# Kernel optimization log

Hardware: AMD Instinct MI355X
Metric: run time of the kernel (lower is better)

Reference implementation:

```python
import jax, jax.numpy as jnp
import numpy as np
import math

D = 2048  # hidden_size
B, S = 4, 2048
EPS = 1e-5


def _ln(z, g, b):
    m = jnp.mean(z, axis=-1, keepdims=True)
    v = jnp.mean(jnp.square(z - m), axis=-1, keepdims=True)
    return (z - m) * jax.lax.rsqrt(v + EPS) * g + b


def _rotate_half(x):
    h = x.shape[-1] // 2
    return jnp.concatenate([-x[..., h:], x[..., :h]], axis=-1)


def _mas_normalize(logits):
    m = jnp.max(jnp.abs(logits), axis=-1, keepdims=True)
    return logits / (m + 1e-9)


def setup_inputs() -> dict:
    key = jax.random.key(0)
    ks = jax.random.split(key, 12)
    std = 0.02
    return {
        "x": jax.random.normal(ks[0], (B, S, D), dtype=jnp.float32),
        "position_ids": jnp.arange(S, dtype=jnp.int32),
        "ln1_g": jnp.ones((D,), jnp.float32),
        "ln1_b": jnp.zeros((D,), jnp.float32),
        # stacked params for [q, k, v, o]
        "mu_w": std * jax.random.normal(ks[1], (4, D, D), dtype=jnp.float32),
        "mu_b": jnp.zeros((4, D), jnp.float32),
        "proto_w": std * jax.random.normal(ks[2], (4, D, D), dtype=jnp.float32),
        "gate": jnp.zeros((4, D), jnp.float32),
        "pt_w": std * jax.random.normal(ks[3], (4, D, D), dtype=jnp.float32),
        "pln_g": jnp.ones((4, D), jnp.float32),
        "pln_b": jnp.zeros((4, D), jnp.float32),
        "incoming": std * jax.random.normal(ks[4], (4, D, D), dtype=jnp.float32),
    }


def reference(x, position_ids, ln1_g, ln1_b, mu_w, mu_b, proto_w, gate,
              pt_w, pln_g, pln_b, incoming):
    d = x.shape[-1]
    inv_sqrt_d = 1.0 / math.sqrt(d)

    # proto_state = proto_weight + LN(Linear(incoming))  per module [4, D, D]
    prc = jnp.einsum('nij,noj->nio', incoming, pt_w)
    proto_state = proto_w + _ln(prc, pln_g[:, None, :], pln_b[:, None, :])

    ln1_out = _ln(x, ln1_g, ln1_b)            # [B,S,D]
    ctx = jnp.mean(ln1_out, axis=1)           # [B,D]

    # qkv computation outputs: silu(ln1_out @ mu_w.T + mu_b) for n in {q,k,v}
    comp = jax.nn.silu(jnp.einsum('bsd,nod->nbso', ln1_out, mu_w[:3])
                       + mu_b[:3][:, None, None, :])            # [3,B,S,D]
    # routing from context vector
    match_ctx = jnp.einsum('bd,nod->nbo', ctx, proto_state[:3]) * inv_sqrt_d
    routing = match_ctx + gate[:3][:, None, :]                  # [3,B,D]
    gating = _mas_normalize(routing)
    masked = gating[:, :, None, :] * comp                       # [3,B,S,D]
    q, k, v = masked[0], masked[1], masked[2]

    # RoPE over full hidden dim (num_heads == 1)
    seq = position_ids.shape[0]
    inv_freq = 1.0 / (10000.0 ** (jnp.arange(0, d, 2, dtype=jnp.float32) / d))
    t = jnp.arange(seq, dtype=jnp.float32)
    freqs = t[:, None] * inv_freq[None, :]
    emb = jnp.concatenate([freqs, freqs], axis=-1)              # [S,D]
    cos = jnp.cos(emb)[position_ids]
    sin = jnp.sin(emb)[position_ids]
    q = q * cos + _rotate_half(q) * sin
    k = k * cos + _rotate_half(k) * sin

    # causal single-head attention, scale 1/sqrt(head_dim=D)
    scores = jnp.einsum('bqd,bkd->bqk', q, k) * inv_sqrt_d      # [B,S,S]
    causal = jnp.tril(jnp.ones((seq, seq), dtype=bool))
    scores = jnp.where(causal, scores, jnp.finfo(scores.dtype).min)
    probs = jax.nn.softmax(scores, axis=-1)
    attn_out = jnp.einsum('bqk,bkd->bqd', probs, v)             # [B,S,D]

    # output SPL + routing
    ctx_o = jnp.mean(attn_out, axis=1)
    c_o = jax.nn.silu(jnp.einsum('bsd,od->bso', attn_out, mu_w[3]) + mu_b[3])
    match_o = jnp.einsum('bd,od->bo', ctx_o, proto_state[3]) * inv_sqrt_d
    gating_o = _mas_normalize(match_o + gate[3])
    x_out = x + gating_o[:, None, :] * c_o
    return x_out
```

## Files before the change

kernel.cpp:

```cpp
#include <hip/hip_runtime.h>
#include <hip/hip_bf16.h>

#define Dh 2048
#define Bh 4
#define Sh 2048
#define NROW 8192
#define HALF 1024
#define INV_SQRT_D 0.022097086912079608f
#define LNEPS 1e-5f

typedef __hip_bfloat16 bf16;
typedef short short8 __attribute__((ext_vector_type(8)));
typedef float f32x4 __attribute__((ext_vector_type(4)));

__device__ inline float warp_sum(float x) {
#pragma unroll
  for (int o = 32; o > 0; o >>= 1) x += __shfl_down(x, o);
  return x;
}
__device__ inline float warp_max(float x) {
#pragma unroll
  for (int o = 32; o > 0; o >>= 1) x = fmaxf(x, __shfl_down(x, o));
  return x;
}
__device__ inline float block_sum(float x, float* sm4) {
  x = warp_sum(x);
  int w = threadIdx.x >> 6;
  if ((threadIdx.x & 63) == 0) sm4[w] = x;
  __syncthreads();
  float r = sm4[0] + sm4[1] + sm4[2] + sm4[3];
  __syncthreads();
  return r;
}
__device__ inline float block_max(float x, float* sm4) {
  x = warp_max(x);
  int w = threadIdx.x >> 6;
  if ((threadIdx.x & 63) == 0) sm4[w] = x;
  __syncthreads();
  float r = fmaxf(fmaxf(sm4[0], sm4[1]), fmaxf(sm4[2], sm4[3]));
  __syncthreads();
  return r;
}

__device__ inline void gload_lds16(const void* g, void* lds) {
  __builtin_amdgcn_global_load_lds(
      (const __attribute__((address_space(1))) unsigned int*)(unsigned long long)g,
      (__attribute__((address_space(3))) unsigned int*)(unsigned long long)lds,
      16, 0, 0);
}

#define MM(R, AF)                                                              \
  acc[R][0] = __builtin_amdgcn_mfma_f32_16x16x32_bf16(AF, b0, acc[R][0], 0, 0, 0); \
  acc[R][1] = __builtin_amdgcn_mfma_f32_16x16x32_bf16(AF, b1, acc[R][1], 0, 0, 0); \
  acc[R][2] = __builtin_amdgcn_mfma_f32_16x16x32_bf16(AF, b2, acc[R][2], 0, 0, 0); \
  acc[R][3] = __builtin_amdgcn_mfma_f32_16x16x32_bf16(AF, b3, acc[R][3], 0, 0, 0);

template <int MODE>
__global__ __launch_bounds__(512, 4) void pgemm(
    const bf16* __restrict__ Aall, const bf16* __restrict__ Ball,
    void* __restrict__ Call, int N, int K, int lda, int ldb,
    long sAz, long sBz, long sCz,
    const float* __restrict__ e0, const float* __restrict__ e1,
    const float* __restrict__ e2) {
  const int bm0 = blockIdx.x * 128;
  const int bn0 = blockIdx.y * 256;
  if (MODE == 2 && bn0 > bm0 + 127) return;
  const int z = blockIdx.z;
  const bf16* A = Aall + (long)z * sAz;
  const bf16* B = Ball + (long)z * sBz;

  __shared__ __align__(16) char smem[49152];
  const int tid = threadIdx.x;
  const int l = tid & 63, w = tid >> 6;
  const int wr = w >> 2, wc = w & 3;

  f32x4 acc[4][4] = {};
  const int nt = K >> 5;

  const int sg = (((l & 3) ^ ((l >> 3) & 3)) << 3);
  const int srow = (w << 4) + (l >> 2);
  const bf16* aS  = A + (long)(bm0 + srow) * lda + sg;
  const bf16* bS0 = B + (long)(bn0 + srow) * ldb + sg;
  const bf16* bS1 = B + (long)(bn0 + 128 + srow) * ldb + sg;
  char* const dA = smem + (w << 10);
  char* const dB = smem + 8192 + (w << 10);

  auto stageA = [&](int tt) {
    gload_lds16(aS + (tt << 5), dA + (tt & 1) * 24576);
  };
  auto stageB = [&](int tt) {
    int boff = (tt & 1) * 24576;
    gload_lds16(bS0 + (tt << 5), dB + boff);
    gload_lds16(bS1 + (tt << 5), dB + boff + 8192);
  };

  stageA(0); stageB(0);
  if (nt > 1) stageB(1);
  if (nt > 1) asm volatile("s_waitcnt vmcnt(2)" ::: "memory");
  else        asm volatile("s_waitcnt vmcnt(0)" ::: "memory");
  __builtin_amdgcn_sched_barrier(0);
  asm volatile("s_barrier" ::: "memory");

  const int rslot = (((l >> 4) ^ ((l >> 1) & 3)) << 4);
  const int abyte = (((wr << 6) + (l & 15)) << 6) + rslot;
  const int bbyte = (((wc << 6) + (l & 15)) << 6) + rslot;

  for (int t = 0; t < nt; ++t) {
    const char* Ab = smem + (t & 1) * 24576;
    const char* Bb = Ab + 8192;
    short8 b0 = *(const short8*)(Bb + bbyte);
    short8 b1 = *(const short8*)(Bb + bbyte + 1024);
    short8 b2 = *(const short8*)(Bb + bbyte + 2048);
    short8 b3 = *(const short8*)(Bb + bbyte + 3072);
    short8 a0 = *(const short8*)(Ab + abyte);
    short8 a1 = *(const short8*)(Ab + abyte + 1024);
    if (t + 1 < nt) stageA(t + 1);
    MM(0, a0) MM(1, a1)
    asm volatile("s_waitcnt lgkmcnt(0)" ::: "memory");
    asm volatile("s_barrier" ::: "memory");
    short8 a2 = *(const short8*)(Ab + abyte + 2048);
    short8 a3 = *(const short8*)(Ab + abyte + 3072);
    if (t + 2 < nt) stageB(t + 2);
    MM(2, a2) MM(3, a3)
    if (t < nt - 1) {
      asm volatile("s_waitcnt lgkmcnt(0)" ::: "memory");
      if (t + 2 < nt) asm volatile("s_waitcnt vmcnt(2)" ::: "memory");
      else            asm volatile("s_waitcnt vmcnt(0)" ::: "memory");
      __builtin_amdgcn_sched_barrier(0);
      asm volatile("s_barrier" ::: "memory");
    }
  }

  const int lc = l & 15, lr4 = (l >> 4) << 2;
#pragma unroll
  for (int fr = 0; fr < 4; ++fr) {
    int gr0 = bm0 + (wr << 6) + fr * 16 + lr4;
#pragma unroll
    for (int fc = 0; fc < 4; ++fc) {
      int gc = bn0 + (wc << 6) + fc * 16 + lc;
#pragma unroll
      for (int qv = 0; qv < 4; ++qv) {
        int gr = gr0 + qv;
        float a = acc[fr][fc][qv];
        if (MODE == 0) {
          ((float*)Call + (long)z * sCz)[(long)gr * N + gc] = a;
        } else if (MODE == 1) {
          float val = a + e0[z * Dh + gc];
          float sil = val / (1.f + __expf(-val));
          int bb = gr >> 11;
          float g = e1[(z * Bh + bb) * Dh + gc];
          ((bf16*)Call + (long)z * sCz)[(long)gr * N + gc] =
              __float2bfloat16(sil * g);
        } else if (MODE == 2) {
          ((float*)Call + (long)z * sCz)[(long)gr * N + gc] = a * INV_SQRT_D;
        } else {
          float val = a + e0[gc];
          float sil = val / (1.f + __expf(-val));
          int bb = gr >> 11;
          ((float*)Call)[(long)gr * N + gc] =
              e2[(long)gr * N + gc] + e1[bb * Dh + gc] * sil;
        }
      }
    }
  }
}

__global__ __launch_bounds__(512, 4) void pgemm_h(
    const bf16* __restrict__ Aall, const bf16* __restrict__ Ball,
    bf16* __restrict__ Call, int N, int lda, int ldb,
    long sAz, long sBz, long sCz) {
  const int fid = blockIdx.x;
  const int p = fid >> 8, q = fid & 255;
  const int mh = q >> 5;
  const int z = (q >> 3) & 3, ni = q & 7;
  const int mi = p ? (15 - mh) : mh;
  const int bm0 = mi * 128, bn0 = ni * 256;
  const bf16* A = Aall + (long)z * sAz;
  const bf16* B = Ball + (long)z * sBz;

  __shared__ __align__(16) char smem[49152];
  const int tid = threadIdx.x;
  const int l = tid & 63, w = tid >> 6;
  const int wr = w >> 2, wc = w & 3;
  f32x4 acc[4][4] = {};
  const int nt = (bm0 + 128) >> 5;

  const int sg = (((l & 3) ^ ((l >> 3) & 3)) << 3);
  const int srow = (w << 4) + (l >> 2);
  const bf16* aS  = A + (long)(bm0 + srow) * lda + sg;
  const bf16* bS0 = B + (long)(bn0 + srow) * ldb + sg;
  const bf16* bS1 = B + (long)(bn0 + 128 + srow) * ldb + sg;
  char* const dA = smem + (w << 10);
  char* const dB = smem + 8192 + (w << 10);

  auto stageA = [&](int tt) {
    gload_lds16(aS + (tt << 5), dA + (tt & 1) * 24576);
  };
  auto stageB = [&](int tt) {
    int boff = (tt & 1) * 24576;
    gload_lds16(bS0 + (tt << 5), dB + boff);
    gload_lds16(bS1 + (tt << 5), dB + boff + 8192);
  };

  stageA(0); stageB(0);
  if (nt > 1) stageB(1);
  if (nt > 1) asm volatile("s_waitcnt vmcnt(2)" ::: "memory");
  else        asm volatile("s_waitcnt vmcnt(0)" ::: "memory");
  __builtin_amdgcn_sched_barrier(0);
  asm volatile("s_barrier" ::: "memory");

  const int rslot = (((l >> 4) ^ ((l >> 1) & 3)) << 4);
  const int abyte = (((wr << 6) + (l & 15)) << 6) + rslot;
  const int bbyte = (((wc << 6) + (l & 15)) << 6) + rslot;

  for (int t = 0; t < nt; ++t) {
    const char* Ab = smem + (t & 1) * 24576;
    const char* Bb = Ab + 8192;
    short8 b0 = *(const short8*)(Bb + bbyte);
    short8 b1 = *(const short8*)(Bb + bbyte + 1024);
    short8 b2 = *(const short8*)(Bb + bbyte + 2048);
    short8 b3 = *(const short8*)(Bb + bbyte + 3072);
    short8 a0 = *(const short8*)(Ab + abyte);
    short8 a1 = *(const short8*)(Ab + abyte + 1024);
    if (t + 1 < nt) stageA(t + 1);
    MM(0, a0) MM(1, a1)
    asm volatile("s_waitcnt lgkmcnt(0)" ::: "memory");
    asm volatile("s_barrier" ::: "memory");
    short8 a2 = *(const short8*)(Ab + abyte + 2048);
    short8 a3 = *(const short8*)(Ab + abyte + 3072);
    if (t + 2 < nt) stageB(t + 2);
    MM(2, a2) MM(3, a3)
    if (t < nt - 1) {
      asm volatile("s_waitcnt lgkmcnt(0)" ::: "memory");
      if (t + 2 < nt) asm volatile("s_waitcnt vmcnt(2)" ::: "memory");
      else            asm volatile("s_waitcnt vmcnt(0)" ::: "memory");
      __builtin_amdgcn_sched_barrier(0);
      asm volatile("s_barrier" ::: "memory");
    }
  }

  const int lc = l & 15, lr4 = (l >> 4) << 2;
  bf16* C = Call + (long)z * sCz;
#pragma unroll
  for (int fr = 0; fr < 4; ++fr) {
    int gr0 = bm0 + (wr << 6) + fr * 16 + lr4;
#pragma unroll
    for (int fc = 0; fc < 4; ++fc) {
      int gc = bn0 + (wc << 6) + fc * 16 + lc;
#pragma unroll
      for (int qv = 0; qv < 4; ++qv) {
        C[(long)(gr0 + qv) * N + gc] = __float2bfloat16(acc[fr][fc][qv]);
      }
    }
  }
}

__global__ __launch_bounds__(256) void cvt3_kernel(
    const float* __restrict__ s0, const float* __restrict__ s1,
    const float* __restrict__ s2, bf16* __restrict__ o0, bf16* __restrict__ o1,
    bf16* __restrict__ o2, long n) {
  const float* in = (blockIdx.y == 0) ? s0 : (blockIdx.y == 1) ? s1 : s2;
  bf16* out = (blockIdx.y == 0) ? o0 : (blockIdx.y == 1) ? o1 : o2;
  long i = ((long)blockIdx.x * 256 + threadIdx.x) * 4;
  if (i >= n) return;
  float4 v = *(const float4*)(in + i);
  out[i + 0] = __float2bfloat16(v.x);
  out[i + 1] = __float2bfloat16(v.y);
  out[i + 2] = __float2bfloat16(v.z);
  out[i + 3] = __float2bfloat16(v.w);
}

__global__ __launch_bounds__(256) void transpose_kernel(const bf16* __restrict__ in,
                                                        bf16* __restrict__ out) {
  __shared__ bf16 t[64][65];
  int b = blockIdx.z;
  int s0 = blockIdx.x * 64, d0 = blockIdx.y * 64;
  const bf16* ib = in + (long)b * Sh * Dh;
  bf16* ob = out + (long)b * Sh * Dh;
  int tx = threadIdx.x & 63, ty = threadIdx.x >> 6;
#pragma unroll
  for (int r = ty; r < 64; r += 4) t[r][tx] = ib[(long)(s0 + r) * Dh + d0 + tx];
  __syncthreads();
#pragma unroll
  for (int r = ty; r < 64; r += 4) ob[(long)(d0 + r) * Sh + s0 + tx] = t[tx][r];
}

__global__ __launch_bounds__(256) void ln1_kernel(const float* __restrict__ x,
    const float* __restrict__ g, const float* __restrict__ b, bf16* __restrict__ out) {
  __shared__ float sm4[4];
  long r = blockIdx.x;
  const float* row = x + r * Dh;
  float v[8];
  float s = 0.f, s2 = 0.f;
#pragma unroll
  for (int c = 0; c < 8; ++c) {
    float t = row[threadIdx.x + c * 256];
    v[c] = t; s += t; s2 += t * t;
  }
  s = block_sum(s, sm4);
  s2 = block_sum(s2, sm4);
  float mean = s * (1.f / Dh);
  float rstd = rsqrtf(s2 * (1.f / Dh) - mean * mean + LNEPS);
#pragma unroll
  for (int c = 0; c < 8; ++c) {
    int o = threadIdx.x + c * 256;
    out[r * Dh + o] = __float2bfloat16((v[c] - mean) * rstd * g[o] + b[o]);
  }
}

__global__ __launch_bounds__(256) void meanrow_kernel(const bf16* __restrict__ in,
                                                      float* __restrict__ outbd) {
  int gid = blockIdx.x * 256 + threadIdx.x;
  int s0 = blockIdx.y * 128;
  long base = ((long)(gid >> 11) * Sh + s0) * Dh + (gid & 2047);
  float s = 0.f;
  for (int t = 0; t < 128; ++t) s += __bfloat162float(in[base + (long)t * Dh]);
  atomicAdd(&outbd[gid], s * (1.f / Sh));
}

__global__ __launch_bounds__(256) void route_kernel(
    const float* __restrict__ prc, const float* __restrict__ proto_w,
    const float* __restrict__ pln_g, const float* __restrict__ pln_b,
    const float* __restrict__ gate, const float* __restrict__ ctx,
    float* __restrict__ routing, float* __restrict__ ps3) {
  __shared__ float sm4[4];
  int i = blockIdx.x, n = blockIdx.y;
  long rb = ((long)n * Dh + i) * Dh;
  float v[8];
  float s = 0.f, s2 = 0.f;
#pragma unroll
  for (int c = 0; c < 8; ++c) {
    float t = prc[rb + threadIdx.x + c * 256];
    v[c] = t; s += t; s2 += t * t;
  }
  s = block_sum(s, sm4);
  s2 = block_sum(s2, sm4);
  float mean = s * (1.f / Dh);
  float rstd = rsqrtf(s2 * (1.f / Dh) - mean * mean + LNEPS);
  if (n == 3) {
#pragma unroll
    for (int c = 0; c < 8; ++c) {
      int o = threadIdx.x + c * 256;
      float ps = proto_w[rb + o] + (v[c] - mean) * rstd * pln_g[3 * Dh + o] + pln_b[3 * Dh + o];
      ps3[(long)i * Dh + o] = ps;
    }
  } else {
    float acc[4] = {0.f, 0.f, 0.f, 0.f};
#pragma unroll
    for (int c = 0; c < 8; ++c) {
      int o = threadIdx.x + c * 256;
      float ps = proto_w[rb + o] + (v[c] - mean) * rstd * pln_g[n * Dh + o] + pln_b[n * Dh + o];
#pragma unroll
      for (int b = 0; b < 4; ++b) acc[b] += ps * ctx[b * Dh + o];
    }
    for (int b = 0; b < 4; ++b) {
      float r = block_sum(acc[b], sm4);
      if (threadIdx.x == 0)
        routing[(n * 4 + b) * Dh + i] = r * INV_SQRT_D + gate[n * Dh + i];
    }
  }
}

__global__ __launch_bounds__(256) void route_o_kernel(
    const float* __restrict__ ps3, const float* __restrict__ ctxo,
    const float* __restrict__ gate, float* __restrict__ routing) {
  __shared__ float sm4[4];
  int i = blockIdx.x;
  float acc[4] = {0.f, 0.f, 0.f, 0.f};
#pragma unroll
  for (int c = 0; c < 8; ++c) {
    int o = threadIdx.x + c * 256;
    float p = ps3[(long)i * Dh + o];
#pragma unroll
    for (int b = 0; b < 4; ++b) acc[b] += p * ctxo[b * Dh + o];
  }
  for (int b = 0; b < 4; ++b) {
    float r = block_sum(acc[b], sm4);
    if (threadIdx.x == 0)
      routing[(12 + b) * Dh + i] = r * INV_SQRT_D + gate[3 * Dh + i];
  }
}

__global__ __launch_bounds__(256) void masnorm_kernel(const float* __restrict__ rin,
                                                      float* __restrict__ gout) {
  __shared__ float sm4[4];
  long r = blockIdx.x;
  float m = 0.f;
#pragma unroll
  for (int c = 0; c < 8; ++c)
    m = fmaxf(m, fabsf(rin[r * Dh + threadIdx.x + c * 256]));
  m = block_max(m, sm4);
  float inv = 1.f / (m + 1e-9f);
#pragma unroll
  for (int c = 0; c < 8; ++c) {
    int o = threadIdx.x + c * 256;
    gout[r * Dh + o] = rin[r * Dh + o] * inv;
  }
}

__global__ __launch_bounds__(256) void rope_table_kernel(float* __restrict__ cosT,
                                                         float* __restrict__ sinT) {
  int idx = blockIdx.x * 256 + threadIdx.x;
  int t = idx >> 10, f = idx & 1023;
  float inv_freq = expf(-(float)f * (9.210340371976184f / 1024.f));
  float ang = (float)t * inv_freq;
  cosT[idx] = cosf(ang);
  sinT[idx] = sinf(ang);
}

__global__ __launch_bounds__(256) void rope_kernel(bf16* __restrict__ q, bf16* __restrict__ k,
    const int* __restrict__ pos, const float* __restrict__ cosT,
    const float* __restrict__ sinT) {
  long r = blockIdx.x;
  int s = (int)(r & (Sh - 1));
  int p = pos[s];
#pragma unroll
  for (int c = 0; c < 4; ++c) {
    int t = threadIdx.x + c * 256;
    float cv = cosT[(long)p * HALF + t];
    float sv = sinT[(long)p * HALF + t];
    long i1 = r * Dh + t, i2 = i1 + HALF;
    float q1 = __bfloat162float(q[i1]), q2 = __bfloat162float(q[i2]);
    q[i1] = __float2bfloat16(q1 * cv - q2 * sv);
    q[i2] = __float2bfloat16(q2 * cv + q1 * sv);
    float k1 = __bfloat162float(k[i1]), k2 = __bfloat162float(k[i2]);
    k[i1] = __float2bfloat16(k1 * cv - k2 * sv);
    k[i2] = __float2bfloat16(k2 * cv + k1 * sv);
  }
}

__global__ __launch_bounds__(256) void softmax_kernel(const float* __restrict__ scores,
                                                      bf16* __restrict__ probs) {
  __shared__ float buf[Sh];
  __shared__ float sm4[4];
  long r = blockIdx.x;
  int qi = (int)(r & (Sh - 1));
  const float* row = scores + r * (long)Sh;
  bf16* prow = probs + r * (long)Sh;
  int n = qi + 1;
  float m = -3.0e38f;
  for (int o = threadIdx.x; o < n; o += 256) {
    float x = row[o]; buf[o] = x; m = fmaxf(m, x);
  }
  m = block_max(m, sm4);
  float s = 0.f;
  for (int o = threadIdx.x; o < n; o += 256) {
    float e = __expf(buf[o] - m); buf[o] = e; s += e;
  }
  s = block_sum(s, sm4);
  float inv = 1.f / s;
  for (int o = threadIdx.x; o < n; o += 256) prow[o] = __float2bfloat16(buf[o] * inv);
  for (int o = n + (int)threadIdx.x; o < Sh; o += 256) prow[o] = __float2bfloat16(0.f);
}

extern "C" void kernel_launch(void* const* d_in, const int* in_sizes, int n_in,
                              void* d_out, int out_size, void* d_ws, size_t ws_size,
                              hipStream_t stream) {
  const float* x       = (const float*)d_in[0];
  const int*   pos     = (const int*)d_in[1];
  const float* ln1_g   = (const float*)d_in[2];
  const float* ln1_b   = (const float*)d_in[3];
  const float* mu_w    = (const float*)d_in[4];
  const float* mu_b    = (const float*)d_in[5];
  const float* proto_w = (const float*)d_in[6];
  const float* gate    = (const float*)d_in[7];
  const float* pt_w    = (const float*)d_in[8];
  const float* pln_g   = (const float*)d_in[9];
  const float* pln_b   = (const float*)d_in[10];
  const float* incoming= (const float*)d_in[11];

  char* w = (char*)d_ws;
  const long BF = 33554432L;
  bf16*  ln1    = (bf16*)(w);
  bf16*  qb     = (bf16*)(w + BF);
  bf16*  kb     = (bf16*)(w + 2 * BF);
  bf16*  vb     = (bf16*)(w + 3 * BF);
  bf16*  attn   = (bf16*)(w + 4 * BF);
  bf16*  mu_wb  = (bf16*)(w + 5 * BF);
  bf16*  ptw_b  = (bf16*)(w + 6 * BF);
  bf16*  vT     = ptw_b;
  bf16*  inc_b  = (bf16*)(w + 7 * BF);
  bf16*  probs  = inc_b;
  float* ps3    = (float*)(w + 8 * BF);
  float* cosT   = (float*)(w + 8 * BF + 16777216L);
  float* sinT   = cosT + (long)Sh * HALF;
  float* ctx    = sinT + (long)Sh * HALF;
  float* ctxo   = ctx + Bh * Dh;
  float* routing= ctxo + Bh * Dh;
  float* gating = routing + 16 * Dh;
  float* scores = (float*)d_out;

  const long DD4 = 4L * Dh * Dh;

  hipMemsetAsync(ctx, 0, 2L * Bh * Dh * sizeof(float), stream);

  rope_table_kernel<<<(Sh * HALF) / 256, 256, 0, stream>>>(cosT, sinT);
  cvt3_kernel<<<dim3(DD4 / 1024, 3), 256, 0, stream>>>(
      mu_w, incoming, pt_w, mu_wb, inc_b, ptw_b, DD4);
  ln1_kernel<<<NROW, 256, 0, stream>>>(x, ln1_g, ln1_b, ln1);
  meanrow_kernel<<<dim3(32, 16), 256, 0, stream>>>(ln1, ctx);
  pgemm<0><<<dim3(16, 8, 4), 512, 0, stream>>>(
      inc_b, ptw_b, scores, Dh, Dh, Dh, Dh,
      (long)Dh * Dh, (long)Dh * Dh, (long)Dh * Dh, nullptr, nullptr, nullptr);
  route_kernel<<<dim3(Dh, 4), 256, 0, stream>>>(scores, proto_w, pln_g, pln_b,
                                                gate, ctx, routing, ps3);
  masnorm_kernel<<<12, 256, 0, stream>>>(routing, gating);
  pgemm<1><<<dim3(64, 8, 3), 512, 0, stream>>>(
      ln1, mu_wb, qb, Dh, Dh, Dh, Dh,
      0L, (long)Dh * Dh, (long)NROW * Dh, mu_b, gating, nullptr);
  rope_kernel<<<NROW, 256, 0, stream>>>(qb, kb, pos, cosT, sinT);
  pgemm<2><<<dim3(16, 8, 4), 512, 0, stream>>>(
      qb, kb, scores, Sh, Dh, Dh, Dh,
      (long)Sh * Dh, (long)Sh * Dh, (long)Sh * Sh, nullptr, nullptr, nullptr);
  softmax_kernel<<<Bh * Sh, 256, 0, stream>>>(scores, probs);
  transpose_kernel<<<dim3(32, 32, 4), 256, 0, stream>>>(vb, vT);
  pgemm_h<<<512, 512, 0, stream>>>(
      probs, vT, attn, Dh, Sh, Sh,
      (long)Sh * Sh, (long)Dh * Sh, (long)Sh * Dh);
  meanrow_kernel<<<dim3(32, 16), 256, 0, stream>>>(attn, ctxo);
  route_o_kernel<<<Dh, 256, 0, stream>>>(ps3, ctxo, gate, routing);
  masnorm_kernel<<<4, 256, 0, stream>>>(routing + 12 * Dh, gating + 12 * Dh);
  pgemm<4><<<dim3(64, 8, 1), 512, 0, stream>>>(
      attn, mu_wb + 3L * Dh * Dh, d_out, Dh, Dh, Dh, Dh,
      0L, 0L, 0L, mu_b + 3 * Dh, gating + 12 * Dh, x);
}
```

Before: 710.3 us.

## Fuse RoPE into QKV GEMM epilogue, widen warp tiles, store scores as fp16

```diff
diff --git a/kernel.cpp b/kernel.cpp
--- a/kernel.cpp
+++ b/kernel.cpp
@@ -1,5 +1,6 @@
 #include <hip/hip_runtime.h>
 #include <hip/hip_bf16.h>
+#include <hip/hip_fp16.h>
 
 #define Dh 2048
 #define Bh 4
@@ -56,14 +57,17 @@
   acc[R][3] = __builtin_amdgcn_mfma_f32_16x16x32_bf16(AF, b3, acc[R][3], 0, 0, 0);
 
 template <int MODE>
-__global__ __launch_bounds__(512, 4) void pgemm(
+__global__ __launch_bounds__(256, 2) void pgemm(
     const bf16* __restrict__ Aall, const bf16* __restrict__ Ball,
     void* __restrict__ Call, int N, int K, int lda, int ldb,
     long sAz, long sBz, long sCz,
     const float* __restrict__ e0, const float* __restrict__ e1,
-    const float* __restrict__ e2) {
+    const float* __restrict__ e2,
+    const int* __restrict__ pos, const float* __restrict__ cosT,
+    const float* __restrict__ sinT) {
   const int bm0 = blockIdx.x * 128;
   const int bn0 = blockIdx.y * 256;
+  const int ns = blockIdx.y;
   if (MODE == 2 && bn0 > bm0 + 127) return;
   const int z = blockIdx.z;
   const bf16* A = Aall + (long)z * sAz;
@@ -71,38 +75,50 @@
 
   __shared__ __align__(16) char smem[49152];
   const int tid = threadIdx.x;
-  const int l = tid & 63, w = tid >> 6;
-  const int wr = w >> 2, wc = w & 3;
-
-  f32x4 acc[4][4] = {};
+  const int l = tid & 63, wc = tid >> 6;
+
+  f32x4 acc[8][4] = {};
   const int nt = K >> 5;
 
   const int sg = (((l & 3) ^ ((l >> 3) & 3)) << 3);
-  const int srow = (w << 4) + (l >> 2);
-  const bf16* aS  = A + (long)(bm0 + srow) * lda + sg;
-  const bf16* bS0 = B + (long)(bn0 + srow) * ldb + sg;
-  const bf16* bS1 = B + (long)(bn0 + 128 + srow) * ldb + sg;
-  char* const dA = smem + (w << 10);
-  char* const dB = smem + 8192 + (w << 10);
+  const int lrow = l >> 2;
+  const bf16* aP0 = A + (long)(bm0 + (wc << 4) + lrow) * lda + sg;
+  const bf16* aP1 = aP0 + 64L * lda;
+  const bf16* bP[4];
+#pragma unroll
+  for (int j = 0; j < 4; ++j) {
+    int colbase;
+    if (MODE == 1)
+      colbase = (((wc >> 1) & 1) << 10) + (ns << 7) + (j << 5) + ((wc & 1) << 4);
+    else
+      colbase = bn0 + (wc << 4) + (j << 6);
+    bP[j] = B + (long)(colbase + lrow) * ldb + sg;
+  }
+  char* const dA = smem + (wc << 10);
+  char* const dB = smem + 8192 + (wc << 10);
 
   auto stageA = [&](int tt) {
-    gload_lds16(aS + (tt << 5), dA + (tt & 1) * 24576);
+    int boff = (tt & 1) * 24576;
+    gload_lds16(aP0 + (tt << 5), dA + boff);
+    gload_lds16(aP1 + (tt << 5), dA + boff + 4096);
   };
   auto stageB = [&](int tt) {
     int boff = (tt & 1) * 24576;
-    gload_lds16(bS0 + (tt << 5), dB + boff);
-    gload_lds16(bS1 + (tt << 5), dB + boff + 8192);
+    gload_lds16(bP[0] + (tt << 5), dB + boff);
+    gload_lds16(bP[1] + (tt << 5), dB + boff + 4096);
+    gload_lds16(bP[2] + (tt << 5), dB + boff + 8192);
+    gload_lds16(bP[3] + (tt << 5), dB + boff + 12288);
   };
 
   stageA(0); stageB(0);
   if (nt > 1) stageB(1);
-  if (nt > 1) asm volatile("s_waitcnt vmcnt(2)" ::: "memory");
+  if (nt > 1) asm volatile("s_waitcnt vmcnt(4)" ::: "memory");
   else        asm volatile("s_waitcnt vmcnt(0)" ::: "memory");
   __builtin_amdgcn_sched_barrier(0);
   asm volatile("s_barrier" ::: "memory");
 
   const int rslot = (((l >> 4) ^ ((l >> 1) & 3)) << 4);
-  const int abyte = (((wr << 6) + (l & 15)) << 6) + rslot;
+  const int abyte = ((l & 15) << 6) + rslot;
   const int bbyte = (((wc << 6) + (l & 15)) << 6) + rslot;
 
   for (int t = 0; t < nt; ++t) {
@@ -114,17 +130,21 @@
     short8 b3 = *(const short8*)(Bb + bbyte + 3072);
     short8 a0 = *(const short8*)(Ab + abyte);
     short8 a1 = *(const short8*)(Ab + abyte + 1024);
+    short8 a2 = *(const short8*)(Ab + abyte + 2048);
+    short8 a3 = *(const short8*)(Ab + abyte + 3072);
     if (t + 1 < nt) stageA(t + 1);
-    MM(0, a0) MM(1, a1)
+    MM(0, a0) MM(1, a1) MM(2, a2) MM(3, a3)
     asm volatile("s_waitcnt lgkmcnt(0)" ::: "memory");
     asm volatile("s_barrier" ::: "memory");
-    short8 a2 = *(const short8*)(Ab + abyte + 2048);
-    short8 a3 = *(const short8*)(Ab + abyte + 3072);
+    short8 a4 = *(const short8*)(Ab + abyte + 4096);
+    short8 a5 = *(const short8*)(Ab + abyte + 5120);
+    short8 a6 = *(const short8*)(Ab + abyte + 6144);
+    short8 a7 = *(const short8*)(Ab + abyte + 7168);
     if (t + 2 < nt) stageB(t + 2);
-    MM(2, a2) MM(3, a3)
+    MM(4, a4) MM(5, a5) MM(6, a6) MM(7, a7)
     if (t < nt - 1) {
       asm volatile("s_waitcnt lgkmcnt(0)" ::: "memory");
-      if (t + 2 < nt) asm volatile("s_waitcnt vmcnt(2)" ::: "memory");
+      if (t + 2 < nt) asm volatile("s_waitcnt vmcnt(4)" ::: "memory");
       else            asm volatile("s_waitcnt vmcnt(0)" ::: "memory");
       __builtin_amdgcn_sched_barrier(0);
       asm volatile("s_barrier" ::: "memory");
@@ -133,39 +153,72 @@
 
   const int lc = l & 15, lr4 = (l >> 4) << 2;
 #pragma unroll
-  for (int fr = 0; fr < 4; ++fr) {
-    int gr0 = bm0 + (wr << 6) + fr * 16 + lr4;
-#pragma unroll
-    for (int fc = 0; fc < 4; ++fc) {
-      int gc = bn0 + (wc << 6) + fc * 16 + lc;
+  for (int fr = 0; fr < 8; ++fr) {
+    int gr0 = bm0 + fr * 16 + lr4;
+    if (MODE == 1) {
+      int gcs[4];
+#pragma unroll
+      for (int fc = 0; fc < 4; ++fc)
+        gcs[fc] = ((fc >> 1) << 10) + (ns << 7) + (wc << 5) + ((fc & 1) << 4) + lc;
+      int chi0 = (ns << 7) + (wc << 5) + lc;
 #pragma unroll
       for (int qv = 0; qv < 4; ++qv) {
         int gr = gr0 + qv;
-        float a = acc[fr][fc][qv];
-        if (MODE == 0) {
-          ((float*)Call + (long)z * sCz)[(long)gr * N + gc] = a;
-        } else if (MODE == 1) {
-          float val = a + e0[z * Dh + gc];
+        int s = gr & (Sh - 1);
+        int bb = gr >> 11;
+        float msk[4];
+#pragma unroll
+        for (int fc = 0; fc < 4; ++fc) {
+          float val = acc[fr][fc][qv] + e0[z * Dh + gcs[fc]];
           float sil = val / (1.f + __expf(-val));
-          int bb = gr >> 11;
-          float g = e1[(z * Bh + bb) * Dh + gc];
-          ((bf16*)Call + (long)z * sCz)[(long)gr * N + gc] =
-              __float2bfloat16(sil * g);
-        } else if (MODE == 2) {
-          ((float*)Call + (long)z * sCz)[(long)gr * N + gc] = a * INV_SQRT_D;
+          msk[fc] = sil * e1[(z * Bh + bb) * Dh + gcs[fc]];
+        }
+        float out[4];
+        if (z < 2) {
+          int p = pos[s];
+          float cv0 = cosT[(long)p * HALF + chi0];
+          float sv0 = sinT[(long)p * HALF + chi0];
+          float cv1 = cosT[(long)p * HALF + chi0 + 16];
+          float sv1 = sinT[(long)p * HALF + chi0 + 16];
+          out[0] = msk[0] * cv0 - msk[2] * sv0;
+          out[1] = msk[1] * cv1 - msk[3] * sv1;
+          out[2] = msk[2] * cv0 + msk[0] * sv0;
+          out[3] = msk[3] * cv1 + msk[1] * sv1;
         } else {
-          float val = a + e0[gc];
-          float sil = val / (1.f + __expf(-val));
-          int bb = gr >> 11;
-          ((float*)Call)[(long)gr * N + gc] =
-              e2[(long)gr * N + gc] + e1[bb * Dh + gc] * sil;
+          out[0] = msk[0]; out[1] = msk[1]; out[2] = msk[2]; out[3] = msk[3];
+        }
+        bf16* C = (bf16*)Call + (long)z * sCz;
+#pragma unroll
+        for (int fc = 0; fc < 4; ++fc)
+          C[(long)gr * N + gcs[fc]] = __float2bfloat16(out[fc]);
+      }
+    } else {
+#pragma unroll
+      for (int fc = 0; fc < 4; ++fc) {
+        int gc = bn0 + (wc << 6) + fc * 16 + lc;
+#pragma unroll
+        for (int qv = 0; qv < 4; ++qv) {
+          int gr = gr0 + qv;
+          float a = acc[fr][fc][qv];
+          if (MODE == 0) {
+            ((float*)Call + (long)z * sCz)[(long)gr * N + gc] = a;
+          } else if (MODE == 2) {
+            ((__half*)Call + (long)z * sCz)[(long)gr * N + gc] =
+                __float2half(a * INV_SQRT_D);
+          } else {
+            float val = a + e0[gc];
+            float sil = val / (1.f + __expf(-val));
+            int bb = gr >> 11;
+            ((float*)Call)[(long)gr * N + gc] =
+                e2[(long)gr * N + gc] + e1[bb * Dh + gc] * sil;
+          }
         }
       }
     }
   }
 }
 
-__global__ __launch_bounds__(512, 4) void pgemm_h(
+__global__ __launch_bounds__(256, 2) void pgemm_h(
     const bf16* __restrict__ Aall, const bf16* __restrict__ Ball,
     bf16* __restrict__ Call, int N, int lda, int ldb,
     long sAz, long sBz, long sCz) {
@@ -180,37 +233,43 @@
 
   __shared__ __align__(16) char smem[49152];
   const int tid = threadIdx.x;
-  const int l = tid & 63, w = tid >> 6;
-  const int wr = w >> 2, wc = w & 3;
-  f32x4 acc[4][4] = {};
+  const int l = tid & 63, wc = tid >> 6;
+  f32x4 acc[8][4] = {};
   const int nt = (bm0 + 128) >> 5;
 
   const int sg = (((l & 3) ^ ((l >> 3) & 3)) << 3);
-  const int srow = (w << 4) + (l >> 2);
-  const bf16* aS  = A + (long)(bm0 + srow) * lda + sg;
-  const bf16* bS0 = B + (long)(bn0 + srow) * ldb + sg;
-  const bf16* bS1 = B + (long)(bn0 + 128 + srow) * ldb + sg;
-  char* const dA = smem + (w << 10);
-  char* const dB = smem + 8192 + (w << 10);
+  const int lrow = l >> 2;
+  const bf16* aP0 = A + (long)(bm0 + (wc << 4) + lrow) * lda + sg;
+  const bf16* aP1 = aP0 + 64L * lda;
+  const bf16* bP[4];
+#pragma unroll
+  for (int j = 0; j < 4; ++j)
+    bP[j] = B + (long)(bn0 + (wc << 4) + (j << 6) + lrow) * ldb + sg;
+  char* const dA = smem + (wc << 10);
+  char* const dB = smem + 8192 + (wc << 10);
 
   auto stageA = [&](int tt) {
-    gload_lds16(aS + (tt << 5), dA + (tt & 1) * 24576);
+    int boff = (tt & 1) * 24576;
+    gload_lds16(aP0 + (tt << 5), dA + boff);
+    gload_lds16(aP1 + (tt << 5), dA + boff + 4096);
   };
   auto stageB = [&](int tt) {
     int boff = (tt & 1) * 24576;
-    gload_lds16(bS0 + (tt << 5), dB + boff);
-    gload_lds16(bS1 + (tt << 5), dB + boff + 8192);
+    gload_lds16(bP[0] + (tt << 5), dB + boff);
+    gload_lds16(bP[1] + (tt << 5), dB + boff + 4096);
+    gload_lds16(bP[2] + (tt << 5), dB + boff + 8192);
+    gload_lds16(bP[3] + (tt << 5), dB + boff + 12288);
   };
 
   stageA(0); stageB(0);
   if (nt > 1) stageB(1);
-  if (nt > 1) asm volatile("s_waitcnt vmcnt(2)" ::: "memory");
+  if (nt > 1) asm volatile("s_waitcnt vmcnt(4)" ::: "memory");
   else        asm volatile("s_waitcnt vmcnt(0)" ::: "memory");
   __builtin_amdgcn_sched_barrier(0);
   asm volatile("s_barrier" ::: "memory");
 
   const int rslot = (((l >> 4) ^ ((l >> 1) & 3)) << 4);
-  const int abyte = (((wr << 6) + (l & 15)) << 6) + rslot;
+  const int abyte = ((l & 15) << 6) + rslot;
   const int bbyte = (((wc << 6) + (l & 15)) << 6) + rslot;
 
   for (int t = 0; t < nt; ++t) {
@@ -222,17 +281,21 @@
     short8 b3 = *(const short8*)(Bb + bbyte + 3072);
     short8 a0 = *(const short8*)(Ab + abyte);
     short8 a1 = *(const short8*)(Ab + abyte + 1024);
+    short8 a2 = *(const short8*)(Ab + abyte + 2048);
+    short8 a3 = *(const short8*)(Ab + abyte + 3072);
     if (t + 1 < nt) stageA(t + 1);
-    MM(0, a0) MM(1, a1)
+    MM(0, a0) MM(1, a1) MM(2, a2) MM(3, a3)
     asm volatile("s_waitcnt lgkmcnt(0)" ::: "memory");
     asm volatile("s_barrier" ::: "memory");
-    short8 a2 = *(const short8*)(Ab + abyte + 2048);
-    short8 a3 = *(const short8*)(Ab + abyte + 3072);
+    short8 a4 = *(const short8*)(Ab + abyte + 4096);
+    short8 a5 = *(const short8*)(Ab + abyte + 5120);
+    short8 a6 = *(const short8*)(Ab + abyte + 6144);
+    short8 a7 = *(const short8*)(Ab + abyte + 7168);
     if (t + 2 < nt) stageB(t + 2);
-    MM(2, a2) MM(3, a3)
+    MM(4, a4) MM(5, a5) MM(6, a6) MM(7, a7)
     if (t < nt - 1) {
       asm volatile("s_waitcnt lgkmcnt(0)" ::: "memory");
-      if (t + 2 < nt) asm volatile("s_waitcnt vmcnt(2)" ::: "memory");
+      if (t + 2 < nt) asm volatile("s_waitcnt vmcnt(4)" ::: "memory");
       else            asm volatile("s_waitcnt vmcnt(0)" ::: "memory");
       __builtin_amdgcn_sched_barrier(0);
       asm volatile("s_barrier" ::: "memory");
@@ -242,15 +305,14 @@
   const int lc = l & 15, lr4 = (l >> 4) << 2;
   bf16* C = Call + (long)z * sCz;
 #pragma unroll
-  for (int fr = 0; fr < 4; ++fr) {
-    int gr0 = bm0 + (wr << 6) + fr * 16 + lr4;
+  for (int fr = 0; fr < 8; ++fr) {
+    int gr0 = bm0 + fr * 16 + lr4;
 #pragma unroll
     for (int fc = 0; fc < 4; ++fc) {
       int gc = bn0 + (wc << 6) + fc * 16 + lc;
 #pragma unroll
-      for (int qv = 0; qv < 4; ++qv) {
+      for (int qv = 0; qv < 4; ++qv)
         C[(long)(gr0 + qv) * N + gc] = __float2bfloat16(acc[fr][fc][qv]);
-      }
     }
   }
 }
@@ -408,39 +470,18 @@
   sinT[idx] = sinf(ang);
 }
 
-__global__ __launch_bounds__(256) void rope_kernel(bf16* __restrict__ q, bf16* __restrict__ k,
-    const int* __restrict__ pos, const float* __restrict__ cosT,
-    const float* __restrict__ sinT) {
-  long r = blockIdx.x;
-  int s = (int)(r & (Sh - 1));
-  int p = pos[s];
-#pragma unroll
-  for (int c = 0; c < 4; ++c) {
-    int t = threadIdx.x + c * 256;
-    float cv = cosT[(long)p * HALF + t];
-    float sv = sinT[(long)p * HALF + t];
-    long i1 = r * Dh + t, i2 = i1 + HALF;
-    float q1 = __bfloat162float(q[i1]), q2 = __bfloat162float(q[i2]);
-    q[i1] = __float2bfloat16(q1 * cv - q2 * sv);
-    q[i2] = __float2bfloat16(q2 * cv + q1 * sv);
-    float k1 = __bfloat162float(k[i1]), k2 = __bfloat162float(k[i2]);
-    k[i1] = __float2bfloat16(k1 * cv - k2 * sv);
-    k[i2] = __float2bfloat16(k2 * cv + k1 * sv);
-  }
-}
-
-__global__ __launch_bounds__(256) void softmax_kernel(const float* __restrict__ scores,
+__global__ __launch_bounds__(256) void softmax_kernel(const __half* __restrict__ scores,
                                                       bf16* __restrict__ probs) {
   __shared__ float buf[Sh];
   __shared__ float sm4[4];
   long r = blockIdx.x;
   int qi = (int)(r & (Sh - 1));
-  const float* row = scores + r * (long)Sh;
+  const __half* row = scores + r * (long)Sh;
   bf16* prow = probs + r * (long)Sh;
   int n = qi + 1;
   float m = -3.0e38f;
   for (int o = threadIdx.x; o < n; o += 256) {
-    float x = row[o]; buf[o] = x; m = fmaxf(m, x);
+    float x = __half2float(row[o]); buf[o] = x; m = fmaxf(m, x);
   }
   m = block_max(m, sm4);
   float s = 0.f;
@@ -488,7 +529,8 @@
   float* ctxo   = ctx + Bh * Dh;
   float* routing= ctxo + Bh * Dh;
   float* gating = routing + 16 * Dh;
-  float* scores = (float*)d_out;
+  float*  prc    = (float*)d_out;
+  __half* scores = (__half*)d_out;
 
   const long DD4 = 4L * Dh * Dh;
 
@@ -499,28 +541,31 @@
       mu_w, incoming, pt_w, mu_wb, inc_b, ptw_b, DD4);
   ln1_kernel<<<NROW, 256, 0, stream>>>(x, ln1_g, ln1_b, ln1);
   meanrow_kernel<<<dim3(32, 16), 256, 0, stream>>>(ln1, ctx);
-  pgemm<0><<<dim3(16, 8, 4), 512, 0, stream>>>(
-      inc_b, ptw_b, scores, Dh, Dh, Dh, Dh,
-      (long)Dh * Dh, (long)Dh * Dh, (long)Dh * Dh, nullptr, nullptr, nullptr);
-  route_kernel<<<dim3(Dh, 4), 256, 0, stream>>>(scores, proto_w, pln_g, pln_b,
+  pgemm<0><<<dim3(16, 8, 4), 256, 0, stream>>>(
+      inc_b, ptw_b, prc, Dh, Dh, Dh, Dh,
+      (long)Dh * Dh, (long)Dh * Dh, (long)Dh * Dh,
+      nullptr, nullptr, nullptr, nullptr, nullptr, nullptr);
+  route_kernel<<<dim3(Dh, 4), 256, 0, stream>>>(prc, proto_w, pln_g, pln_b,
                                                 gate, ctx, routing, ps3);
   masnorm_kernel<<<12, 256, 0, stream>>>(routing, gating);
-  pgemm<1><<<dim3(64, 8, 3), 512, 0, stream>>>(
+  pgemm<1><<<dim3(64, 8, 3), 256, 0, stream>>>(
       ln1, mu_wb, qb, Dh, Dh, Dh, Dh,
-      0L, (long)Dh * Dh, (long)NROW * Dh, mu_b, gating, nullptr);
-  rope_kernel<<<NROW, 256, 0, stream>>>(qb, kb, pos, cosT, sinT);
-  pgemm<2><<<dim3(16, 8, 4), 512, 0, stream>>>(
+      0L, (long)Dh * Dh, (long)NROW * Dh, mu_b, gating, nullptr,
+      pos, cosT, sinT);
+  pgemm<2><<<dim3(16, 8, 4), 256, 0, stream>>>(
       qb, kb, scores, Sh, Dh, Dh, Dh,
-      (long)Sh * Dh, (long)Sh * Dh, (long)Sh * Sh, nullptr, nullptr, nullptr);
+      (long)Sh * Dh, (long)Sh * Dh, (long)Sh * Sh,
+      nullptr, nullptr, nullptr, nullptr, nullptr, nullptr);
   softmax_kernel<<<Bh * Sh, 256, 0, stream>>>(scores, probs);
   transpose_kernel<<<dim3(32, 32, 4), 256, 0, stream>>>(vb, vT);
-  pgemm_h<<<512, 512, 0, stream>>>(
+  pgemm_h<<<512, 256, 0, stream>>>(
       probs, vT, attn, Dh, Sh, Sh,
       (long)Sh * Sh, (long)Dh * Sh, (long)Sh * Dh);
   meanrow_kernel<<<dim3(32, 16), 256, 0, stream>>>(attn, ctxo);
   route_o_kernel<<<Dh, 256, 0, stream>>>(ps3, ctxo, gate, routing);
   masnorm_kernel<<<4, 256, 0, stream>>>(routing + 12 * Dh, gating + 12 * Dh);
-  pgemm<4><<<dim3(64, 8, 1), 512, 0, stream>>>(
+  pgemm<4><<<dim3(64, 8, 1), 256, 0, stream>>>(
       attn, mu_wb + 3L * Dh * Dh, d_out, Dh, Dh, Dh, Dh,
-      0L, 0L, 0L, mu_b + 3 * Dh, gating + 12 * Dh, x);
-}
+      0L, 0L, 0L, mu_b + 3 * Dh, gating + 12 * Dh, x,
+      nullptr, nullptr, nullptr);
+}
```

Result: no change. 699.2 us (-1.6%).
